# Performance work log

Hardware: AMD Instinct MI355X
Metric: run time of the kernel (lower is better)

Reference implementation:

```python
import jax, jax.numpy as jnp
import numpy as np

N_NODES = 50000


def setup_inputs() -> dict:
    key = jax.random.key(0)
    ks = jax.random.split(key, 10)
    B, N, D, H, O = 2, N_NODES, 128, 128, 10
    x = jax.random.normal(ks[0], (B, N, D), dtype=jnp.float32)
    edge_index = jax.random.randint(ks[1], (2, 800000), 0, N, dtype=jnp.int32)
    s = lambda fan_in: 1.0 / np.sqrt(fan_in)
    W  = jax.random.uniform(ks[2], (D, H), jnp.float32, -s(D), s(D))
    b  = jnp.zeros((H,), jnp.float32)
    W1 = jax.random.uniform(ks[3], (H, H // 2), jnp.float32, -s(H), s(H))
    b1 = jnp.zeros((H // 2,), jnp.float32)
    W2 = jax.random.uniform(ks[4], (H // 2, H // 4), jnp.float32, -s(H // 2), s(H // 2))
    b2 = jnp.zeros((H // 4,), jnp.float32)
    W3 = jax.random.uniform(ks[5], (H // 4, O), jnp.float32, -s(H // 4), s(H // 4))
    b3 = jnp.zeros((O,), jnp.float32)
    return {"x": x, "edge_index": edge_index, "W": W, "b": b,
            "W1": W1, "b1": b1, "W2": W2, "b2": b2, "W3": W3, "b3": b3}


def reference(x, edge_index, W, b, W1, b1, W2, b2, W3, b3):
    # GraphConvolution (Kipf): support = x @ W; out[dst] += support[src]; + b
    src, dst = edge_index[0], edge_index[1]
    support = jnp.einsum("bnd,dh->bnh", x, W)          # [B, N, H]
    msgs = support[:, src, :]                            # [B, E, H] gather
    agg = jnp.zeros_like(support).at[:, dst, :].add(msgs)  # scatter-add
    h = jax.nn.gelu(agg + b, approximate=False)          # GELU (torch default erf)
    # dropout is identity at inference (training=False)
    h = jax.nn.relu(jnp.einsum("bnh,hk->bnk", h, W1) + b1)
    h = jax.nn.relu(jnp.einsum("bnk,km->bnm", h, W2) + b2)
    h = jnp.einsum("bnm,mo->bno", h, W3) + b3            # [B, N, O]
    return h.mean(axis=1)                                # [B, O]
```

## Files before the change

### kernel.cpp

```cpp
#include <hip/hip_runtime.h>
#include <math.h>

#define NN 50000
#define DD 128
#define HH 128
#define L1 64
#define L2 32
#define OO 10

typedef short v8s __attribute__((ext_vector_type(8)));
typedef float v4f __attribute__((ext_vector_type(4)));

__device__ __forceinline__ float bf2f_lo(unsigned u) { return __uint_as_float(u << 16); }
__device__ __forceinline__ float bf2f_hi(unsigned u) { return __uint_as_float(u & 0xffff0000u); }
__device__ __forceinline__ unsigned short f2bf(float f) {
    unsigned u = __float_as_uint(f);
    return (unsigned short)((u + 0x7fffu + ((u >> 16) & 1u)) >> 16);
}
__device__ __forceinline__ float gelu_f(float v) {
    return 0.5f * v * (1.f + erff(v * 0.70710678118654752f));
}

__global__ __launch_bounds__(256) void k_wprep(
    const float* __restrict__ W, const float* __restrict__ W1,
    const float* __restrict__ W2, unsigned short* __restrict__ wtb,
    unsigned short* __restrict__ w1tb, unsigned short* __restrict__ w2tb)
{
    int i = blockIdx.x * 256 + threadIdx.x;
    if (i < 128 * 136) {
        int n = i / 136, k = i % 136;
        wtb[i] = (k < DD) ? f2bf(W[k * HH + n]) : (unsigned short)0;
    } else if (i < 128 * 136 + 64 * 136) {
        int j = i - 128 * 136;
        int n = j / 136, k = j % 136;
        w1tb[j] = (k < HH) ? f2bf(W1[k * L1 + n]) : (unsigned short)0;
    } else if (i < 128 * 136 + 64 * 136 + 32 * 72) {
        int j = i - (128 * 136 + 64 * 136);
        int n = j / 72, k = j % 72;
        w2tb[j] = (k < L1) ? f2bf(W2[k * L2 + n]) : (unsigned short)0;
    }
}

__global__ __launch_bounds__(512, 4) void k_support(
    const float* __restrict__ x, const unsigned short* __restrict__ wtb,
    unsigned short* __restrict__ supb, int rows,
    const int* __restrict__ ei, int* __restrict__ counts, int E)
{
    __shared__ __align__(16) unsigned short xs[128 * 136];
    __shared__ __align__(16) unsigned short wt[128 * 136];
    const int tid = threadIdx.x;
    const int row0 = blockIdx.x * 128;

    for (int u = tid * 4; u < 128 * 136; u += 2048)
        *(uint2*)(&wt[u]) = *(const uint2*)(wtb + u);
    for (int u = tid * 4; u < 128 * DD; u += 2048) {
        const int r = u >> 7, c = u & 127;
        float4 v = make_float4(0.f, 0.f, 0.f, 0.f);
        if (row0 + r < rows) v = *(const float4*)(x + (size_t)(row0 + r) * DD + c);
        ushort4 o;
        o.x = f2bf(v.x); o.y = f2bf(v.y); o.z = f2bf(v.z); o.w = f2bf(v.w);
        *(ushort4*)(&xs[r * 136 + c]) = o;
    }

    {
        const int chunk = (E + gridDim.x - 1) / gridDim.x;
        const int e0 = blockIdx.x * chunk;
        const int e1 = min(e0 + chunk, E);
        for (int e = e0 + tid; e < e1; e += 512)
            atomicAdd(&counts[ei[(size_t)E + e]], 1);
    }
    __syncthreads();

    const int lane = tid & 63;
    const int w = tid >> 6;
    const int m0 = w * 16;
    const int lm = lane & 15;
    const int q  = lane >> 4;

    v4f acc[8];
    #pragma unroll
    for (int i = 0; i < 8; ++i) acc[i] = (v4f)(0.f);

    #pragma unroll
    for (int ks = 0; ks < 4; ++ks) {
        const int k0 = ks * 32 + q * 8;
        const v8s af = *(const v8s*)(&xs[(m0 + lm) * 136 + k0]);
        #pragma unroll
        for (int ct = 0; ct < 8; ++ct) {
            const v8s bf = *(const v8s*)(&wt[(ct * 16 + lm) * 136 + k0]);
            acc[ct] = __builtin_amdgcn_mfma_f32_16x16x32_bf16(af, bf, acc[ct], 0, 0, 0);
        }
    }

    #pragma unroll
    for (int ct = 0; ct < 8; ++ct) {
        const int col = ct * 16 + lm;
        #pragma unroll
        for (int r = 0; r < 4; ++r) {
            const int rowg = row0 + m0 + q * 4 + r;
            if (rowg < rows) {
                const int b = (rowg >= NN) ? 1 : 0;
                const int n = rowg - b * NN;
                supb[((size_t)n * 2 + b) * HH + col] = f2bf(acc[ct][r]);
            }
        }
    }
}

__global__ __launch_bounds__(1024) void k_scan1(
    const int* __restrict__ counts, int* __restrict__ offsets,
    int* __restrict__ blksum, int n)
{
    __shared__ int wsum[16], woff[16];
    const int tid = threadIdx.x, lane = tid & 63, wv = tid >> 6;
    const int i = blockIdx.x * 1024 + tid;
    int v = (i < n) ? counts[i] : 0;
    int x = v;
    #pragma unroll
    for (int d = 1; d < 64; d <<= 1) { int t = __shfl_up(x, d); if (lane >= d) x += t; }
    if (lane == 63) wsum[wv] = x;
    __syncthreads();
    if (wv == 0 && lane < 16) {
        int y = wsum[lane];
        #pragma unroll
        for (int d = 1; d < 16; d <<= 1) { int t = __shfl_up(y, d); if (lane >= d) y += t; }
        woff[lane] = y - wsum[lane];
        if (lane == 15) blksum[blockIdx.x] = y;
    }
    __syncthreads();
    if (i < n) offsets[i] = woff[wv] + (x - v);
}

__global__ __launch_bounds__(1024) void k_scan2(
    int* __restrict__ offsets, const int* __restrict__ blksum, int nblk, int n)
{
    __shared__ int base_sh, tot_sh;
    const int tid = threadIdx.x, lane = tid & 63, wv = tid >> 6;
    if (wv == 0) {
        int v = (lane < nblk) ? blksum[lane] : 0;
        int x = v;
        #pragma unroll
        for (int d = 1; d < 64; d <<= 1) { int t = __shfl_up(x, d); if (lane >= d) x += t; }
        int incl = __shfl(x, blockIdx.x);
        int own  = __shfl(v, blockIdx.x);
        int tot  = __shfl(x, nblk - 1);
        if (lane == 0) { base_sh = incl - own; tot_sh = tot; }
    }
    __syncthreads();
    const int i = blockIdx.x * 1024 + tid;
    if (i < n) offsets[i] += base_sh;
    if (blockIdx.x == nblk - 1 && tid == 0) offsets[n] = tot_sh;
}

__global__ __launch_bounds__(256) void k_bucket(
    const int* __restrict__ ei, const int* __restrict__ offsets,
    int* __restrict__ cursor, int* __restrict__ ss, int E)
{
    int e = blockIdx.x * 256 + threadIdx.x;
    if (e < E) {
        int d = ei[E + e];
        int pos = offsets[d] + atomicAdd(&cursor[d], 1);
        ss[pos] = ei[e];
    }
}

__global__ __launch_bounds__(256) void k_agg(
    const unsigned short* __restrict__ supb, const int* __restrict__ offsets,
    const int* __restrict__ ss, unsigned short* __restrict__ aggb, int nn)
{
    const int tid = threadIdx.x;
    const int lane = tid & 63;
    const int wv = tid >> 6;
    const int d = blockIdx.x * 4 + wv;
    if (d >= nn) return;
    const unsigned short* sp = supb + lane * 4;
    const int s0 = offsets[d], s1 = offsets[d + 1];
    float4 a = make_float4(0.f, 0.f, 0.f, 0.f);
    float4 a2 = make_float4(0.f, 0.f, 0.f, 0.f);
    int i = s0;
    for (; i + 4 <= s1; i += 4) {
        const int sA = ss[i], sB = ss[i + 1], sC = ss[i + 2], sD = ss[i + 3];
        const uint2 rA = *(const uint2*)(sp + (size_t)sA * 256);
        const uint2 rB = *(const uint2*)(sp + (size_t)sB * 256);
        const uint2 rC = *(const uint2*)(sp + (size_t)sC * 256);
        const uint2 rD = *(const uint2*)(sp + (size_t)sD * 256);
        a.x  += bf2f_lo(rA.x); a.y  += bf2f_hi(rA.x); a.z  += bf2f_lo(rA.y); a.w  += bf2f_hi(rA.y);
        a2.x += bf2f_lo(rB.x); a2.y += bf2f_hi(rB.x); a2.z += bf2f_lo(rB.y); a2.w += bf2f_hi(rB.y);
        a.x  += bf2f_lo(rC.x); a.y  += bf2f_hi(rC.x); a.z  += bf2f_lo(rC.y); a.w  += bf2f_hi(rC.y);
        a2.x += bf2f_lo(rD.x); a2.y += bf2f_hi(rD.x); a2.z += bf2f_lo(rD.y); a2.w += bf2f_hi(rD.y);
    }
    for (; i < s1; ++i) {
        const uint2 r = *(const uint2*)(sp + (size_t)ss[i] * 256);
        a.x += bf2f_lo(r.x); a.y += bf2f_hi(r.x); a.z += bf2f_lo(r.y); a.w += bf2f_hi(r.y);
    }
    a.x += a2.x; a.y += a2.y; a.z += a2.z; a.w += a2.w;
    ushort4 o;
    o.x = f2bf(a.x); o.y = f2bf(a.y); o.z = f2bf(a.z); o.w = f2bf(a.w);
    *(ushort4*)(aggb + (size_t)d * 256 + lane * 4) = o;
}

__global__ __launch_bounds__(512, 6) void k_mlp(
    const unsigned short* __restrict__ aggb, const float* __restrict__ b0v,
    const unsigned short* __restrict__ w1tb, const float* __restrict__ b1v,
    const unsigned short* __restrict__ w2tb, const float* __restrict__ b2v,
    float* __restrict__ partials, int srows)
{
    __shared__ __align__(16) unsigned short wt1[64 * 136];
    __shared__ __align__(16) unsigned short wt2[32 * 72];
    __shared__ __align__(16) unsigned char upool[64 * 136 * 2];
    __shared__ __align__(16) unsigned short h1b[64 * 72];
    __shared__ float b0s[DD], b1s[L1], b2s[L2];
    __shared__ float oacc[64];
    unsigned short* hsb = (unsigned short*)upool;
    float* h2p = (float*)upool;

    const int tid = threadIdx.x;
    const int row0 = blockIdx.x * 64;

    for (int u = tid * 4; u < 64 * 136; u += 2048)
        *(uint2*)(&wt1[u]) = *(const uint2*)(w1tb + u);
    for (int u = tid * 4; u < 32 * 72; u += 2048)
        *(uint2*)(&wt2[u]) = *(const uint2*)(w2tb + u);
    if (tid < DD) b0s[tid] = b0v[tid];
    if (tid < L1) b1s[tid] = b1v[tid];
    if (tid < L2) b2s[tid] = b2v[tid];
    if (tid < 64) oacc[tid] = 0.f;

    for (int u = tid * 8; u < 64 * DD; u += 4096) {
        const int r = u >> 7, c = u & 127;
        uint4 raw = make_uint4(0, 0, 0, 0);
        if (row0 + r < srows) raw = *(const uint4*)(aggb + (size_t)(row0 + r) * HH + c);
        float v[8];
        v[0] = bf2f_lo(raw.x) + b0s[c + 0]; v[1] = bf2f_hi(raw.x) + b0s[c + 1];
        v[2] = bf2f_lo(raw.y) + b0s[c + 2]; v[3] = bf2f_hi(raw.y) + b0s[c + 3];
        v[4] = bf2f_lo(raw.z) + b0s[c + 4]; v[5] = bf2f_hi(raw.z) + b0s[c + 5];
        v[6] = bf2f_lo(raw.w) + b0s[c + 6]; v[7] = bf2f_hi(raw.w) + b0s[c + 7];
        ushort4 o0, o1;
        o0.x = f2bf(gelu_f(v[0])); o0.y = f2bf(gelu_f(v[1]));
        o0.z = f2bf(gelu_f(v[2])); o0.w = f2bf(gelu_f(v[3]));
        o1.x = f2bf(gelu_f(v[4])); o1.y = f2bf(gelu_f(v[5]));
        o1.z = f2bf(gelu_f(v[6])); o1.w = f2bf(gelu_f(v[7]));
        *(ushort4*)(&hsb[r * 136 + c]) = o0;
        *(ushort4*)(&hsb[r * 136 + c + 4]) = o1;
    }
    __syncthreads();

    const int lane = tid & 63;
    const int w = tid >> 6;
    const int lm = lane & 15;
    const int q = lane >> 4;
    const int r1 = (w & 3) * 16;

    {
        const int c1 = (w >> 2) * 32;
        v4f a1[2];
        a1[0] = (v4f)(0.f); a1[1] = (v4f)(0.f);
        #pragma unroll
        for (int ks = 0; ks < 4; ++ks) {
            const int k0 = ks * 32 + q * 8;
            const v8s af = *(const v8s*)(&hsb[(r1 + lm) * 136 + k0]);
            #pragma unroll
            for (int ct = 0; ct < 2; ++ct) {
                const v8s bf = *(const v8s*)(&wt1[(c1 + ct * 16 + lm) * 136 + k0]);
                a1[ct] = __builtin_amdgcn_mfma_f32_16x16x32_bf16(af, bf, a1[ct], 0, 0, 0);
            }
        }
        #pragma unroll
        for (int ct = 0; ct < 2; ++ct) {
            const int col = c1 + ct * 16 + lm;
            const float bias = b1s[col];
            #pragma unroll
            for (int r = 0; r < 4; ++r)
                h1b[(r1 + q * 4 + r) * 72 + col] = f2bf(fmaxf(a1[ct][r] + bias, 0.f));
        }
    }
    __syncthreads();

    {
        const int c2 = (w >> 2) * 16;
        v4f a2 = (v4f)(0.f);
        #pragma unroll
        for (int ks = 0; ks < 2; ++ks) {
            const int k0 = ks * 32 + q * 8;
            const v8s af = *(const v8s*)(&h1b[(r1 + lm) * 72 + k0]);
            const v8s bf = *(const v8s*)(&wt2[(c2 + lm) * 72 + k0]);
            a2 = __builtin_amdgcn_mfma_f32_16x16x32_bf16(af, bf, a2, 0, 0, 0);
        }
        const int col = c2 + lm;
        const float bias = b2s[col];
        #pragma unroll
        for (int r = 0; r < 4; ++r)
            h2p[(r1 + q * 4 + r) * 36 + col] = fmaxf(a2[r] + bias, 0.f);
    }
    __syncthreads();

    {
        const int c = tid & 31;
        const int g = tid >> 5;
        float p0 = 0.f, p1 = 0.f;
        #pragma unroll
        for (int i = 0; i < 4; ++i) {
            const int r = g * 4 + i;
            if (row0 + r < srows) {
                const float v = h2p[r * 36 + c];
                if (r & 1) p1 += v; else p0 += v;
            }
        }
        if (p0 != 0.f) atomicAdd(&oacc[c], p0);
        if (p1 != 0.f) atomicAdd(&oacc[32 + c], p1);
    }
    __syncthreads();
    if (tid < 64) partials[(size_t)blockIdx.x * 64 + tid] = oacc[tid];
}

__global__ __launch_bounds__(256) void k_scatter(
    const int* __restrict__ ei, const unsigned short* __restrict__ supb,
    float* __restrict__ aggf, int E)
{
    const int tid = threadIdx.x;
    const int eg = tid >> 6;
    const int lane = tid & 63;
    const int e = blockIdx.x * 4 + eg;
    if (e >= E) return;
    const int src = ei[e];
    const int dst = ei[E + e];
    const uint2 r = *(const uint2*)(supb + (size_t)src * 256 + lane * 4);
    float* ap = aggf + (size_t)dst * 256 + lane * 4;
    unsafeAtomicAdd(ap + 0, bf2f_lo(r.x));
    unsafeAtomicAdd(ap + 1, bf2f_hi(r.x));
    unsafeAtomicAdd(ap + 2, bf2f_lo(r.y));
    unsafeAtomicAdd(ap + 3, bf2f_hi(r.y));
}

__global__ __launch_bounds__(256) void k_cvt(
    const float* __restrict__ in, unsigned short* __restrict__ outb, int n)
{
    int i = blockIdx.x * 256 + threadIdx.x;
    if (i < n) outb[i] = f2bf(in[i]);
}

__global__ __launch_bounds__(256) void k_reduce(
    const float* __restrict__ partials, float* __restrict__ accum, int nblk)
{
    __shared__ float lsum[4][64];
    const int t = threadIdx.x & 63;
    const int w = threadIdx.x >> 6;
    float s = 0.f;
    for (int g = blockIdx.x * 4 + w; g < nblk; g += gridDim.x * 4)
        s += partials[(size_t)g * 64 + t];
    lsum[w][t] = s;
    __syncthreads();
    if (threadIdx.x < 64) {
        const float v = lsum[0][t] + lsum[1][t] + lsum[2][t] + lsum[3][t];
        unsafeAtomicAdd(&accum[t], v);
    }
}

__global__ __launch_bounds__(64) void k_final(
    const float* __restrict__ accum, const float* __restrict__ W3,
    const float* __restrict__ b3v, float* __restrict__ out)
{
    const int tid = threadIdx.x;
    if (tid < 2 * OO) {
        const int b = tid / OO, o = tid % OO;
        float acc = b3v[o];
        const float inv = 1.0f / (float)NN;
        #pragma unroll
        for (int j = 0; j < L2; ++j) acc += (accum[b * 32 + j] * inv) * W3[j * OO + o];
        out[tid] = acc;
    }
}

extern "C" void kernel_launch(void* const* d_in, const int* in_sizes, int n_in,
                              void* d_out, int out_size, void* d_ws, size_t ws_size,
                              hipStream_t stream) {
    const float* x  = (const float*)d_in[0];
    const int*   ei = (const int*)d_in[1];
    const float* W  = (const float*)d_in[2];
    const float* b0 = (const float*)d_in[3];
    const float* W1 = (const float*)d_in[4];
    const float* b1 = (const float*)d_in[5];
    const float* W2 = (const float*)d_in[6];
    const float* b2 = (const float*)d_in[7];
    const float* W3 = (const float*)d_in[8];
    const float* b3 = (const float*)d_in[9];
    float* out = (float*)d_out;

    const int E = in_sizes[1] / 2;
    const int rows = 2 * NN;
    const int nblk = (rows + 63) / 64;
    const int nsb = (NN + 1023) / 1024;
    const int wpn = 128 * 136 + 64 * 136 + 32 * 72;

    unsigned short* supb = (unsigned short*)d_ws;
    unsigned short* aggb = supb + (size_t)rows * HH;
    float* partials = (float*)(aggb + (size_t)rows * HH);
    float* accum    = partials + (size_t)nblk * 64;
    int*   counts   = (int*)(accum + 64);
    int*   cursor   = counts + NN;
    int*   offsets  = cursor + NN;
    int*   blksum   = offsets + NN + 1;
    unsigned short* wtb  = (unsigned short*)(blksum + 64);
    unsigned short* w1tb = wtb + 128 * 136;
    unsigned short* w2tb = w1tb + 64 * 136;
    int*   ss       = (int*)(w2tb + 32 * 72);
    float* aggf     = (float*)(ss + E);
    const size_t need_csr = ((size_t)rows * HH * 2 + wpn) * sizeof(unsigned short)
                      + ((size_t)nblk * 64 + 64) * sizeof(float)
                      + ((size_t)NN * 3 + 1 + 64 + E) * sizeof(int);
    const size_t need_fb = need_csr + (size_t)rows * HH * sizeof(float);

    if (ws_size >= need_csr && nsb <= 64) {
        hipMemsetAsync(accum, 0, (64 + 2 * (size_t)NN) * sizeof(int), stream);
        k_wprep<<<dim3((wpn + 255) / 256), dim3(256), 0, stream>>>(W, W1, W2, wtb, w1tb, w2tb);
        k_support<<<dim3((rows + 127) / 128), dim3(512), 0, stream>>>(x, wtb, supb, rows, ei, counts, E);
        k_scan1<<<dim3(nsb), dim3(1024), 0, stream>>>(counts, offsets, blksum, NN);
        k_scan2<<<dim3(nsb), dim3(1024), 0, stream>>>(offsets, blksum, nsb, NN);
        k_bucket<<<dim3((E + 255) / 256), dim3(256), 0, stream>>>(ei, offsets, cursor, ss, E);
        k_agg<<<dim3((NN + 3) / 4), dim3(256), 0, stream>>>(supb, offsets, ss, aggb, NN);
        k_mlp<<<dim3(nblk), dim3(512), 0, stream>>>(aggb, b0, w1tb, b1, w2tb, b2, partials, rows);
    } else if (ws_size >= need_fb) {
        hipMemsetAsync(accum, 0, 64 * sizeof(float), stream);
        hipMemsetAsync(aggf, 0, (size_t)rows * HH * sizeof(float), stream);
        k_wprep<<<dim3((wpn + 255) / 256), dim3(256), 0, stream>>>(W, W1, W2, wtb, w1tb, w2tb);
        k_support<<<dim3((rows + 127) / 128), dim3(512), 0, stream>>>(x, wtb, supb, rows, ei, counts, 0);
        k_scatter<<<dim3((E + 3) / 4), dim3(256), 0, stream>>>(ei, supb, aggf, E);
        k_cvt<<<dim3((rows * HH + 255) / 256), dim3(256), 0, stream>>>(aggf, aggb, rows * HH);
        k_mlp<<<dim3(nblk), dim3(512), 0, stream>>>(aggb, b0, w1tb, b1, w2tb, b2, partials, rows);
    }

    k_reduce<<<dim3(64), dim3(256), 0, stream>>>(partials, accum, nblk);
    k_final<<<dim3(1), dim3(64), 0, stream>>>(accum, W3, b3, out);
}
```

Measured before the change: 280.6 us.

## Aggregate raw features first and fuse the W projection into the MLP kernel

Uses linearity (A·X)·W = A·(X·W) to drop the separate support GEMM kernel. x is converted to bf16 in a node-interleaved layout, the neighbour sum runs on raw features, and the 128x128 W matmul is done inside k_mlp before bias and GELU, with W fragments read straight from global memory. This removes one GEMM pass and its bf16 intermediate write. In exchange the MLP kernel does more work and adds extra syncs, and bf16 rounding now happens before the projection instead of after it.

```diff
diff --git a/kernel.cpp b/kernel.cpp
--- a/kernel.cpp
+++ b/kernel.cpp
@@ -41,70 +41,25 @@
     }
 }
 
-__global__ __launch_bounds__(512, 4) void k_support(
-    const float* __restrict__ x, const unsigned short* __restrict__ wtb,
-    unsigned short* __restrict__ supb, int rows,
+__global__ __launch_bounds__(256) void k_xcvt(
+    const float* __restrict__ x, unsigned short* __restrict__ xb,
     const int* __restrict__ ei, int* __restrict__ counts, int E)
 {
-    __shared__ __align__(16) unsigned short xs[128 * 136];
-    __shared__ __align__(16) unsigned short wt[128 * 136];
-    const int tid = threadIdx.x;
-    const int row0 = blockIdx.x * 128;
-
-    for (int u = tid * 4; u < 128 * 136; u += 2048)
-        *(uint2*)(&wt[u]) = *(const uint2*)(wtb + u);
-    for (int u = tid * 4; u < 128 * DD; u += 2048) {
-        const int r = u >> 7, c = u & 127;
-        float4 v = make_float4(0.f, 0.f, 0.f, 0.f);
-        if (row0 + r < rows) v = *(const float4*)(x + (size_t)(row0 + r) * DD + c);
+    const int gid = blockIdx.x * 256 + threadIdx.x;
+    const int stride = gridDim.x * 256;
+    const int HALF = NN * 32;
+    for (int idx = gid; idx < 2 * HALF; idx += stride) {
+        const int b = (idx >= HALF) ? 1 : 0;
+        const int j = idx - b * HALF;
+        const int n = j >> 5;
+        const int c4 = j & 31;
+        const float4 v = *(const float4*)(x + ((size_t)b * NN + n) * DD + c4 * 4);
         ushort4 o;
         o.x = f2bf(v.x); o.y = f2bf(v.y); o.z = f2bf(v.z); o.w = f2bf(v.w);
-        *(ushort4*)(&xs[r * 136 + c]) = o;
-    }
-
-    {
-        const int chunk = (E + gridDim.x - 1) / gridDim.x;
-        const int e0 = blockIdx.x * chunk;
-        const int e1 = min(e0 + chunk, E);
-        for (int e = e0 + tid; e < e1; e += 512)
-            atomicAdd(&counts[ei[(size_t)E + e]], 1);
-    }
-    __syncthreads();
-
-    const int lane = tid & 63;
-    const int w = tid >> 6;
-    const int m0 = w * 16;
-    const int lm = lane & 15;
-    const int q  = lane >> 4;
-
-    v4f acc[8];
-    #pragma unroll
-    for (int i = 0; i < 8; ++i) acc[i] = (v4f)(0.f);
-
-    #pragma unroll
-    for (int ks = 0; ks < 4; ++ks) {
-        const int k0 = ks * 32 + q * 8;
-        const v8s af = *(const v8s*)(&xs[(m0 + lm) * 136 + k0]);
-        #pragma unroll
-        for (int ct = 0; ct < 8; ++ct) {
-            const v8s bf = *(const v8s*)(&wt[(ct * 16 + lm) * 136 + k0]);
-            acc[ct] = __builtin_amdgcn_mfma_f32_16x16x32_bf16(af, bf, acc[ct], 0, 0, 0);
-        }
-    }
-
-    #pragma unroll
-    for (int ct = 0; ct < 8; ++ct) {
-        const int col = ct * 16 + lm;
-        #pragma unroll
-        for (int r = 0; r < 4; ++r) {
-            const int rowg = row0 + m0 + q * 4 + r;
-            if (rowg < rows) {
-                const int b = (rowg >= NN) ? 1 : 0;
-                const int n = rowg - b * NN;
-                supb[((size_t)n * 2 + b) * HH + col] = f2bf(acc[ct][r]);
-            }
-        }
-    }
+        *(ushort4*)(xb + ((size_t)n * 2 + b) * DD + c4 * 4) = o;
+    }
+    for (int e = gid; e < E; e += stride)
+        atomicAdd(&counts[ei[(size_t)E + e]], 1);
 }
 
 __global__ __launch_bounds__(1024) void k_scan1(
@@ -165,7 +120,7 @@
 }
 
 __global__ __launch_bounds__(256) void k_agg(
-    const unsigned short* __restrict__ supb, const int* __restrict__ offsets,
+    const unsigned short* __restrict__ xb, const int* __restrict__ offsets,
     const int* __restrict__ ss, unsigned short* __restrict__ aggb, int nn)
 {
     const int tid = threadIdx.x;
@@ -173,7 +128,7 @@
     const int wv = tid >> 6;
     const int d = blockIdx.x * 4 + wv;
     if (d >= nn) return;
-    const unsigned short* sp = supb + lane * 4;
+    const unsigned short* sp = xb + lane * 4;
     const int s0 = offsets[d], s1 = offsets[d + 1];
     float4 a = make_float4(0.f, 0.f, 0.f, 0.f);
     float4 a2 = make_float4(0.f, 0.f, 0.f, 0.f);
@@ -200,7 +155,8 @@
 }
 
 __global__ __launch_bounds__(512, 6) void k_mlp(
-    const unsigned short* __restrict__ aggb, const float* __restrict__ b0v,
+    const unsigned short* __restrict__ aggb, const unsigned short* __restrict__ wtb,
+    const float* __restrict__ b0v,
     const unsigned short* __restrict__ w1tb, const float* __restrict__ b1v,
     const unsigned short* __restrict__ w2tb, const float* __restrict__ b2v,
     float* __restrict__ partials, int srows)
@@ -211,6 +167,7 @@
     __shared__ __align__(16) unsigned short h1b[64 * 72];
     __shared__ float b0s[DD], b1s[L1], b2s[L2];
     __shared__ float oacc[64];
+    unsigned short* xa  = (unsigned short*)upool;
     unsigned short* hsb = (unsigned short*)upool;
     float* h2p = (float*)upool;
 
@@ -230,18 +187,7 @@
         const int r = u >> 7, c = u & 127;
         uint4 raw = make_uint4(0, 0, 0, 0);
         if (row0 + r < srows) raw = *(const uint4*)(aggb + (size_t)(row0 + r) * HH + c);
-        float v[8];
-        v[0] = bf2f_lo(raw.x) + b0s[c + 0]; v[1] = bf2f_hi(raw.x) + b0s[c + 1];
-        v[2] = bf2f_lo(raw.y) + b0s[c + 2]; v[3] = bf2f_hi(raw.y) + b0s[c + 3];
-        v[4] = bf2f_lo(raw.z) + b0s[c + 4]; v[5] = bf2f_hi(raw.z) + b0s[c + 5];
-        v[6] = bf2f_lo(raw.w) + b0s[c + 6]; v[7] = bf2f_hi(raw.w) + b0s[c + 7];
-        ushort4 o0, o1;
-        o0.x = f2bf(gelu_f(v[0])); o0.y = f2bf(gelu_f(v[1]));
-        o0.z = f2bf(gelu_f(v[2])); o0.w = f2bf(gelu_f(v[3]));
-        o1.x = f2bf(gelu_f(v[4])); o1.y = f2bf(gelu_f(v[5]));
-        o1.z = f2bf(gelu_f(v[6])); o1.w = f2bf(gelu_f(v[7]));
-        *(ushort4*)(&hsb[r * 136 + c]) = o0;
-        *(ushort4*)(&hsb[r * 136 + c + 4]) = o1;
+        *(uint4*)(&xa[r * 136 + c]) = raw;
     }
     __syncthreads();
 
@@ -250,6 +196,35 @@
     const int lm = lane & 15;
     const int q = lane >> 4;
     const int r1 = (w & 3) * 16;
+
+    {
+        const int c0 = (w >> 2) * 64;
+        const unsigned short* wcol = wtb + (size_t)(c0 + lm) * 136;
+        v4f acc[4];
+        #pragma unroll
+        for (int i = 0; i < 4; ++i) acc[i] = (v4f)(0.f);
+        #pragma unroll
+        for (int ks = 0; ks < 4; ++ks) {
+            const int k0 = ks * 32 + q * 8;
+            const v8s af = *(const v8s*)(&xa[(r1 + lm) * 136 + k0]);
+            #pragma unroll
+            for (int ct = 0; ct < 4; ++ct) {
+                const v8s bf = *(const v8s*)(wcol + ct * 16 * 136 + k0);
+                acc[ct] = __builtin_amdgcn_mfma_f32_16x16x32_bf16(af, bf, acc[ct], 0, 0, 0);
+            }
+        }
+        __syncthreads();
+
+        #pragma unroll
+        for (int ct = 0; ct < 4; ++ct) {
+            const int col = c0 + ct * 16 + lm;
+            const float bias = b0s[col];
+            #pragma unroll
+            for (int r = 0; r < 4; ++r)
+                hsb[(r1 + q * 4 + r) * 136 + col] = f2bf(gelu_f(acc[ct][r] + bias));
+        }
+    }
+    __syncthreads();
 
     {
         const int c1 = (w >> 2) * 32;
@@ -286,6 +261,7 @@
             const v8s bf = *(const v8s*)(&wt2[(c2 + lm) * 72 + k0]);
             a2 = __builtin_amdgcn_mfma_f32_16x16x32_bf16(af, bf, a2, 0, 0, 0);
         }
+        __syncthreads();
         const int col = c2 + lm;
         const float bias = b2s[col];
         #pragma unroll
@@ -314,7 +290,7 @@
 }
 
 __global__ __launch_bounds__(256) void k_scatter(
-    const int* __restrict__ ei, const unsigned short* __restrict__ supb,
+    const int* __restrict__ ei, const unsigned short* __restrict__ xb,
     float* __restrict__ aggf, int E)
 {
     const int tid = threadIdx.x;
@@ -324,7 +300,7 @@
     if (e >= E) return;
     const int src = ei[e];
     const int dst = ei[E + e];
-    const uint2 r = *(const uint2*)(supb + (size_t)src * 256 + lane * 4);
+    const uint2 r = *(const uint2*)(xb + (size_t)src * 256 + lane * 4);
     float* ap = aggf + (size_t)dst * 256 + lane * 4;
     unsafeAtomicAdd(ap + 0, bf2f_lo(r.x));
     unsafeAtomicAdd(ap + 1, bf2f_hi(r.x));
@@ -392,8 +368,8 @@
     const int nsb = (NN + 1023) / 1024;
     const int wpn = 128 * 136 + 64 * 136 + 32 * 72;
 
-    unsigned short* supb = (unsigned short*)d_ws;
-    unsigned short* aggb = supb + (size_t)rows * HH;
+    unsigned short* xb   = (unsigned short*)d_ws;
+    unsigned short* aggb = xb + (size_t)rows * HH;
     float* partials = (float*)(aggb + (size_t)rows * HH);
     float* accum    = partials + (size_t)nblk * 64;
     int*   counts   = (int*)(accum + 64);
@@ -413,20 +389,20 @@
     if (ws_size >= need_csr && nsb <= 64) {
         hipMemsetAsync(accum, 0, (64 + 2 * (size_t)NN) * sizeof(int), stream);
         k_wprep<<<dim3((wpn + 255) / 256), dim3(256), 0, stream>>>(W, W1, W2, wtb, w1tb, w2tb);
-        k_support<<<dim3((rows + 127) / 128), dim3(512), 0, stream>>>(x, wtb, supb, rows, ei, counts, E);
+        k_xcvt<<<dim3(2048), dim3(256), 0, stream>>>(x, xb, ei, counts, E);
         k_scan1<<<dim3(nsb), dim3(1024), 0, stream>>>(counts, offsets, blksum, NN);
         k_scan2<<<dim3(nsb), dim3(1024), 0, stream>>>(offsets, blksum, nsb, NN);
         k_bucket<<<dim3((E + 255) / 256), dim3(256), 0, stream>>>(ei, offsets, cursor, ss, E);
-        k_agg<<<dim3((NN + 3) / 4), dim3(256), 0, stream>>>(supb, offsets, ss, aggb, NN);
-        k_mlp<<<dim3(nblk), dim3(512), 0, stream>>>(aggb, b0, w1tb, b1, w2tb, b2, partials, rows);
+        k_agg<<<dim3((NN + 3) / 4), dim3(256), 0, stream>>>(xb, offsets, ss, aggb, NN);
+        k_mlp<<<dim3(nblk), dim3(512), 0, stream>>>(aggb, wtb, b0, w1tb, b1, w2tb, b2, partials, rows);
     } else if (ws_size >= need_fb) {
         hipMemsetAsync(accum, 0, 64 * sizeof(float), stream);
         hipMemsetAsync(aggf, 0, (size_t)rows * HH * sizeof(float), stream);
         k_wprep<<<dim3((wpn + 255) / 256), dim3(256), 0, stream>>>(W, W1, W2, wtb, w1tb, w2tb);
-        k_support<<<dim3((rows + 127) / 128), dim3(512), 0, stream>>>(x, wtb, supb, rows, ei, counts, 0);
-        k_scatter<<<dim3((E + 3) / 4), dim3(256), 0, stream>>>(ei, supb, aggf, E);
+        k_xcvt<<<dim3(2048), dim3(256), 0, stream>>>(x, xb, ei, counts, 0);
+        k_scatter<<<dim3((E + 3) / 4), dim3(256), 0, stream>>>(ei, xb, aggf, E);
         k_cvt<<<dim3((rows * HH + 255) / 256), dim3(256), 0, stream>>>(aggf, aggb, rows * HH);
-        k_mlp<<<dim3(nblk), dim3(512), 0, stream>>>(aggb, b0, w1tb, b1, w2tb, b2, partials, rows);
+        k_mlp<<<dim3(nblk), dim3(512), 0, stream>>>(aggb, wtb, b0, w1tb, b1, w2tb, b2, partials, rows);
     }
 
     k_reduce<<<dim3(64), dim3(256), 0, stream>>>(partials, accum, nblk);
```

After: 281.8 us. About the same (+0.4%).
